# Optimization experiments

Measured on AMD Instinct MI355X. Metric: run time of the kernel, lower is better.

## Reference

```python
import jax, jax.numpy as jnp
import numpy as np

N = 50000
E = 800000
D_IN = 128
D_HID = 128
D_OUT = 64


def setup_inputs() -> dict:
    key = jax.random.key(0)
    ks = jax.random.split(key, 9)
    x = jax.random.normal(ks[0], (N, D_IN), dtype=jnp.float32)
    edge_index = jax.random.randint(ks[1], (2, E), 0, N, dtype=jnp.int64)
    # PyG SAGEConv params: lin_l (neighbor path, with bias), lin_r (root path, no bias)
    s1 = 1.0 / np.sqrt(D_IN)
    s2 = 1.0 / np.sqrt(D_HID)
    return {
        "x": x,
        "edge_index": edge_index,
        "W1l": jax.random.uniform(ks[2], (D_IN, D_HID), jnp.float32, -s1, s1),
        "b1": jax.random.uniform(ks[3], (D_HID,), jnp.float32, -s1, s1),
        "W1r": jax.random.uniform(ks[4], (D_IN, D_HID), jnp.float32, -s1, s1),
        "W2l": jax.random.uniform(ks[5], (D_HID, D_OUT), jnp.float32, -s2, s2),
        "b2": jax.random.uniform(ks[6], (D_OUT,), jnp.float32, -s2, s2),
        "W2r": jax.random.uniform(ks[7], (D_HID, D_OUT), jnp.float32, -s2, s2),
    }


def _sage_conv(h, src, dst, Wl, b, Wr, n_nodes):
    # mean-aggregate source features onto target nodes
    msg = h[src]  # [E, d] gather
    summed = jax.ops.segment_sum(msg, dst, num_segments=n_nodes)
    cnt = jax.ops.segment_sum(jnp.ones((src.shape[0],), h.dtype), dst, num_segments=n_nodes)
    mean = summed / jnp.maximum(cnt, 1.0)[:, None]
    return mean @ Wl + b + h @ Wr


def reference(x, edge_index, W1l, b1, W1r, W2l, b2, W2r):
    src, dst = edge_index[0], edge_index[1]
    n = x.shape[0]
    h = jax.nn.relu(_sage_conv(x, src, dst, W1l, b1, W1r, n))
    # dropout is identity in eval mode
    return _sage_conv(h, src, dst, W2l, b2, W2r, n)
```

## Files before the change

### kernel.cpp

```cpp
#include <hip/hip_runtime.h>

#define NN   50000
#define NE   800000
#define CAP  48
#define NPG  6250
#define EPB  3125
#define SEG  576

#define BIN_BLOCKS  256
#define CVT_BLOCKS  (3125 + 128)
#define ZERO_BLOCKS 196
#define SCAT_BLOCKS 2048

typedef __attribute__((ext_vector_type(8))) short bf16x8;
typedef __attribute__((ext_vector_type(4))) float f32x4;

__device__ __forceinline__ unsigned short f2b(float f) {
    unsigned int u = __builtin_bit_cast(unsigned int, f);
    u += 0x7FFFu + ((u >> 16) & 1u);
    return (unsigned short)(u >> 16);
}
__device__ __forceinline__ float b2f_lo(unsigned int u) {
    return __builtin_bit_cast(float, u << 16);
}
__device__ __forceinline__ float b2f_hi(unsigned int u) {
    return __builtin_bit_cast(float, u & 0xFFFF0000u);
}

__global__ __launch_bounds__(256) void prep_kernel(const int* __restrict__ src,
                                                   const int* __restrict__ dst,
                                                   int* __restrict__ bcnt,
                                                   unsigned* __restrict__ stage,
                                                   const float* __restrict__ x,
                                                   const float* __restrict__ W1l,
                                                   const float* __restrict__ W1r,
                                                   const float* __restrict__ W2l,
                                                   const float* __restrict__ W2r,
                                                   unsigned short* __restrict__ xb,
                                                   unsigned short* __restrict__ Bt1,
                                                   unsigned short* __restrict__ Bt2,
                                                   int* __restrict__ cursor) {
    if (blockIdx.x < BIN_BLOCKS) {
        __shared__ int cnt[16][8];
        __shared__ int repoff[16][8];
        const int tid = threadIdx.x;
        const int b   = blockIdx.x;
        const int r   = tid >> 4;
        if (tid < 128) ((int*)cnt)[tid] = 0;
        __syncthreads();

        unsigned recs[13], metas[13];
#pragma unroll
        for (int it = 0; it < 13; ++it) {
            const int i = it * 256 + tid;
            metas[it] = 0xFFFFFFFFu;
            if (i < EPB) {
                const int e = b * EPB + i;
                const int s = src[e], d = dst[e];
                const int g = d / NPG;
                const int dloc = d - g * NPG;
                const int slot = atomicAdd(&cnt[r][g], 1);
                recs[it]  = ((unsigned)dloc << 16) | (unsigned)s;
                metas[it] = ((unsigned)r << 20) | ((unsigned)g << 16) | (unsigned)slot;
            }
        }
        __syncthreads();
        if (tid < 8) {
            int off = 0;
#pragma unroll
            for (int rr = 0; rr < 16; ++rr) { repoff[rr][tid] = off; off += cnt[rr][tid]; }
            bcnt[tid * 256 + b] = off;
        }
        __syncthreads();
#pragma unroll
        for (int it = 0; it < 13; ++it) {
            if (metas[it] != 0xFFFFFFFFu) {
                const int rr   = metas[it] >> 20;
                const int g    = (metas[it] >> 16) & 7;
                const int slot = metas[it] & 0xFFFF;
                const int pos  = repoff[rr][g] + slot;
                if (pos < SEG) stage[((g << 8) + b) * SEG + pos] = recs[it];
            }
        }
    } else if (blockIdx.x < BIN_BLOCKS + 3125) {
        int i = (blockIdx.x - BIN_BLOCKS) * 256 + threadIdx.x;
        const float4* p = reinterpret_cast<const float4*>(x) + (size_t)i * 2;
        float4 a = p[0], b = p[1];
        uint4 u;
        u.x = (unsigned)f2b(a.x) | ((unsigned)f2b(a.y) << 16);
        u.y = (unsigned)f2b(a.z) | ((unsigned)f2b(a.w) << 16);
        u.z = (unsigned)f2b(b.x) | ((unsigned)f2b(b.y) << 16);
        u.w = (unsigned)f2b(b.z) | ((unsigned)f2b(b.w) << 16);
        reinterpret_cast<uint4*>(xb)[i] = u;
    } else if (blockIdx.x < BIN_BLOCKS + CVT_BLOCKS) {
        int t = (blockIdx.x - BIN_BLOCKS - 3125) * 256 + threadIdx.x;
        if (t < 32768) {
            int c = t >> 8, k = t & 255;
            float v = (k < 128) ? W1l[k * 128 + c] : W1r[(k - 128) * 128 + c];
            Bt1[c * 256 + k] = f2b(v);
        }
        if (t < 16384) {
            int c = t >> 7, k = t & 127;
            float v = (c < 64) ? W2l[k * 64 + c] : W2r[k * 64 + (c - 64)];
            Bt2[c * 128 + k] = f2b(v);
        }
    } else {
        int i = (blockIdx.x - BIN_BLOCKS - CVT_BLOCKS) * 256 + threadIdx.x;
        if (i < NN) cursor[i] = 0;
    }
}

__global__ __launch_bounds__(256) void scatter_kernel(const int* __restrict__ bcnt,
                                                      const unsigned* __restrict__ stage,
                                                      int* __restrict__ cursor,
                                                      int* __restrict__ col) {
    const int g = blockIdx.x & 7;
    const int b = blockIdx.x >> 3;
    int cnt = bcnt[g * 256 + b];
    if (cnt > SEG) cnt = SEG;
    const unsigned* sp = stage + (size_t)((g << 8) + b) * SEG;
    const int n0 = g * NPG;
    for (int i = threadIdx.x; i < cnt; i += 256) {
        unsigned rec = sp[i];
        int d = n0 + (int)(rec >> 16);
        int p = atomicAdd(&cursor[d], 1);
        if (p < CAP) col[d * CAP + p] = (int)(rec & 0xFFFFu);
    }
}

__global__ __launch_bounds__(256) void agg_gemm1(const unsigned short* __restrict__ xb,
                                                 const int* __restrict__ cursor,
                                                 const int* __restrict__ col,
                                                 const unsigned short* __restrict__ Bt1,
                                                 const float* __restrict__ bias,
                                                 unsigned short* __restrict__ hb) {
    constexpr int LDA = 264;
    __shared__ unsigned short As[64 * LDA];

    const int base = blockIdx.x * 64;
    const int tid  = threadIdx.x;
    const int l    = tid & 15;
    const int sub  = tid >> 4;

    const uint4* fp = reinterpret_cast<const uint4*>(xb);

    for (int gq = 0; gq < 4; ++gq) {
        const int r  = gq * 16 + sub;
        const int gn = base + r;
        float a0 = 0.f, a1 = 0.f, a2 = 0.f, a3 = 0.f,
              a4 = 0.f, a5 = 0.f, a6 = 0.f, a7 = 0.f;
        uint4 xrow = make_uint4(0, 0, 0, 0);
        if (gn < NN) {
            int len = cursor[gn];
            len = (len > CAP) ? CAP : len;
            const int4* cp = reinterpret_cast<const int4*>(col + gn * CAP);
            int j = 0;
            for (; j + 4 <= len; j += 4) {
                int4 c4 = cp[j >> 2];
                uint4 v0 = fp[c4.x * 16 + l];
                uint4 v1 = fp[c4.y * 16 + l];
                uint4 v2 = fp[c4.z * 16 + l];
                uint4 v3 = fp[c4.w * 16 + l];
                a0 += (b2f_lo(v0.x) + b2f_lo(v1.x)) + (b2f_lo(v2.x) + b2f_lo(v3.x));
                a1 += (b2f_hi(v0.x) + b2f_hi(v1.x)) + (b2f_hi(v2.x) + b2f_hi(v3.x));
                a2 += (b2f_lo(v0.y) + b2f_lo(v1.y)) + (b2f_lo(v2.y) + b2f_lo(v3.y));
                a3 += (b2f_hi(v0.y) + b2f_hi(v1.y)) + (b2f_hi(v2.y) + b2f_hi(v3.y));
                a4 += (b2f_lo(v0.z) + b2f_lo(v1.z)) + (b2f_lo(v2.z) + b2f_lo(v3.z));
                a5 += (b2f_hi(v0.z) + b2f_hi(v1.z)) + (b2f_hi(v2.z) + b2f_hi(v3.z));
                a6 += (b2f_lo(v0.w) + b2f_lo(v1.w)) + (b2f_lo(v2.w) + b2f_lo(v3.w));
                a7 += (b2f_hi(v0.w) + b2f_hi(v1.w)) + (b2f_hi(v2.w) + b2f_hi(v3.w));
            }
            for (; j < len; ++j) {
                uint4 v0 = fp[col[gn * CAP + j] * 16 + l];
                a0 += b2f_lo(v0.x);  a1 += b2f_hi(v0.x);
                a2 += b2f_lo(v0.y);  a3 += b2f_hi(v0.y);
                a4 += b2f_lo(v0.z);  a5 += b2f_hi(v0.z);
                a6 += b2f_lo(v0.w);  a7 += b2f_hi(v0.w);
            }
            const float inv = 1.0f / fmaxf((float)len, 1.0f);
            a0 *= inv; a1 *= inv; a2 *= inv; a3 *= inv;
            a4 *= inv; a5 *= inv; a6 *= inv; a7 *= inv;
            xrow = fp[gn * 16 + l];
        }
        uint4 u;
        u.x = (unsigned)f2b(a0) | ((unsigned)f2b(a1) << 16);
        u.y = (unsigned)f2b(a2) | ((unsigned)f2b(a3) << 16);
        u.z = (unsigned)f2b(a4) | ((unsigned)f2b(a5) << 16);
        u.w = (unsigned)f2b(a6) | ((unsigned)f2b(a7) << 16);
        *reinterpret_cast<uint4*>(&As[r * LDA + l * 8])       = u;
        *reinterpret_cast<uint4*>(&As[r * LDA + 128 + l * 8]) = xrow;
    }
    __syncthreads();

    const int wid  = tid >> 6, lane = tid & 63;
    const int lr   = lane & 15;
    const int lk   = (lane >> 4) * 8;

    f32x4 acc[4][2];
#pragma unroll
    for (int t = 0; t < 4; ++t) {
        acc[t][0] = (f32x4){0.f, 0.f, 0.f, 0.f};
        acc[t][1] = (f32x4){0.f, 0.f, 0.f, 0.f};
    }

    for (int ks = 0; ks < 8; ++ks) {
        const int k = ks * 32 + lk;
        bf16x8 b0 = *reinterpret_cast<const bf16x8*>(Bt1 + (size_t)(wid * 32 + lr) * 256 + k);
        bf16x8 b1 = *reinterpret_cast<const bf16x8*>(Bt1 + (size_t)(wid * 32 + 16 + lr) * 256 + k);
#pragma unroll
        for (int t = 0; t < 4; ++t) {
            bf16x8 a = *reinterpret_cast<const bf16x8*>(&As[(t * 16 + lr) * LDA + k]);
            acc[t][0] = __builtin_amdgcn_mfma_f32_16x16x32_bf16(a, b0, acc[t][0], 0, 0, 0);
            acc[t][1] = __builtin_amdgcn_mfma_f32_16x16x32_bf16(a, b1, acc[t][1], 0, 0, 0);
        }
    }

    const int ccol = lane & 15;
    const int ri   = (lane >> 4) * 4;
#pragma unroll
    for (int t = 0; t < 4; ++t) {
#pragma unroll
        for (int f = 0; f < 2; ++f) {
            const int colg = wid * 32 + f * 16 + ccol;
            const float bv = bias[colg];
#pragma unroll
            for (int i = 0; i < 4; ++i) {
                const int gn = base + t * 16 + ri + i;
                if (gn < NN) {
                    hb[(size_t)gn * 128 + colg] = f2b(fmaxf(acc[t][f][i] + bv, 0.f));
                }
            }
        }
    }
}

template <int DB>
__global__ __launch_bounds__(256) void agg_kernel(const unsigned short* __restrict__ feat,
                                                  const int* __restrict__ cursor,
                                                  const int* __restrict__ col,
                                                  float* outf) {
    constexpr int TPN = DB / 8;
    constexpr int NPB = 256 / TPN;
    const int n = blockIdx.x * NPB + threadIdx.x / TPN;
    const int l = threadIdx.x % TPN;
    if (n >= NN) return;
    int len = cursor[n];
    len = (len > CAP) ? CAP : len;
    float a0 = 0.f, a1 = 0.f, a2 = 0.f, a3 = 0.f, a4 = 0.f, a5 = 0.f, a6 = 0.f, a7 = 0.f;
    const uint4* fp = reinterpret_cast<const uint4*>(feat);
    const int4*  cp = reinterpret_cast<const int4*>(col + n * CAP);

    int j = 0;
    for (; j + 4 <= len; j += 4) {
        int4 c4 = cp[j >> 2];
        uint4 v0 = fp[c4.x * TPN + l];
        uint4 v1 = fp[c4.y * TPN + l];
        uint4 v2 = fp[c4.z * TPN + l];
        uint4 v3 = fp[c4.w * TPN + l];
        a0 += (b2f_lo(v0.x) + b2f_lo(v1.x)) + (b2f_lo(v2.x) + b2f_lo(v3.x));
        a1 += (b2f_hi(v0.x) + b2f_hi(v1.x)) + (b2f_hi(v2.x) + b2f_hi(v3.x));
        a2 += (b2f_lo(v0.y) + b2f_lo(v1.y)) + (b2f_lo(v2.y) + b2f_lo(v3.y));
        a3 += (b2f_hi(v0.y) + b2f_hi(v1.y)) + (b2f_hi(v2.y) + b2f_hi(v3.y));
        a4 += (b2f_lo(v0.z) + b2f_lo(v1.z)) + (b2f_lo(v2.z) + b2f_lo(v3.z));
        a5 += (b2f_hi(v0.z) + b2f_hi(v1.z)) + (b2f_hi(v2.z) + b2f_hi(v3.z));
        a6 += (b2f_lo(v0.w) + b2f_lo(v1.w)) + (b2f_lo(v2.w) + b2f_lo(v3.w));
        a7 += (b2f_hi(v0.w) + b2f_hi(v1.w)) + (b2f_hi(v2.w) + b2f_hi(v3.w));
    }
    for (; j < len; ++j) {
        uint4 v0 = fp[col[n * CAP + j] * TPN + l];
        a0 += b2f_lo(v0.x);  a1 += b2f_hi(v0.x);
        a2 += b2f_lo(v0.y);  a3 += b2f_hi(v0.y);
        a4 += b2f_lo(v0.z);  a5 += b2f_hi(v0.z);
        a6 += b2f_lo(v0.w);  a7 += b2f_hi(v0.w);
    }
    const float inv = 1.0f / fmaxf((float)len, 1.0f);
    a0 *= inv; a1 *= inv; a2 *= inv; a3 *= inv;
    a4 *= inv; a5 *= inv; a6 *= inv; a7 *= inv;
    const float4* ap = reinterpret_cast<const float4*>(outf + (size_t)n * DB) + l * 2;
    float4 b0 = ap[0], b1 = ap[1];
    float4 o0 = make_float4(a0 + b0.x, a1 + b0.y, a2 + b0.z, a3 + b0.w);
    float4 o1 = make_float4(a4 + b1.x, a5 + b1.y, a6 + b1.z, a7 + b1.w);
    float4* op = reinterpret_cast<float4*>(outf + (size_t)n * DB) + l * 2;
    op[0] = o0; op[1] = o1;
}

__global__ __launch_bounds__(256) void gemm2_kernel(const unsigned short* __restrict__ A0,
                                                    const unsigned short* __restrict__ Bt,
                                                    const float* __restrict__ bias,
                                                    unsigned short* __restrict__ outb,
                                                    float* __restrict__ outf) {
    constexpr int K   = 128;
    constexpr int LDK = K + 8;
    __shared__ unsigned short Bs[128 * LDK];

    const int tid = threadIdx.x;
    for (int idx = tid; idx < 128 * (K / 8); idx += 256) {
        int c = idx / (K / 8), kc = idx % (K / 8);
        uint4 v = *reinterpret_cast<const uint4*>(Bt + (size_t)c * K + kc * 8);
        *reinterpret_cast<uint4*>(&Bs[c * LDK + kc * 8]) = v;
    }
    __syncthreads();

    const int base = blockIdx.x * 64;
    const int wid  = tid >> 6, lane = tid & 63;
    const int lr   = lane & 15;
    const int lk   = (lane >> 4) * 8;

    f32x4 acc[4][2];
#pragma unroll
    for (int t = 0; t < 4; ++t) {
        acc[t][0] = (f32x4){0.f, 0.f, 0.f, 0.f};
        acc[t][1] = (f32x4){0.f, 0.f, 0.f, 0.f};
    }

    for (int ks = 0; ks < K / 32; ++ks) {
        const int k = ks * 32 + lk;
        bf16x8 b0 = *reinterpret_cast<const bf16x8*>(&Bs[(wid * 32 + lr) * LDK + k]);
        bf16x8 b1 = *reinterpret_cast<const bf16x8*>(&Bs[(wid * 32 + 16 + lr) * LDK + k]);
#pragma unroll
        for (int t = 0; t < 4; ++t) {
            const int row = base + t * 16 + lr;
            uint4 av = make_uint4(0, 0, 0, 0);
            if (row < NN) av = *reinterpret_cast<const uint4*>(A0 + (size_t)row * 128 + k);
            bf16x8 a = *reinterpret_cast<const bf16x8*>(&av);
            acc[t][0] = __builtin_amdgcn_mfma_f32_16x16x32_bf16(a, b0, acc[t][0], 0, 0, 0);
            acc[t][1] = __builtin_amdgcn_mfma_f32_16x16x32_bf16(a, b1, acc[t][1], 0, 0, 0);
        }
    }

    const int ccol = lane & 15;
    const int ri   = (lane >> 4) * 4;
#pragma unroll
    for (int t = 0; t < 4; ++t) {
#pragma unroll
        for (int f = 0; f < 2; ++f) {
            const int colg = wid * 32 + f * 16 + ccol;
#pragma unroll
            for (int i = 0; i < 4; ++i) {
                const int gn = base + t * 16 + ri + i;
                if (gn < NN) {
                    float v = acc[t][f][i];
                    if (colg < 64) outb[(size_t)gn * 64 + colg] = f2b(v);
                    else           outf[(size_t)gn * 64 + (colg - 64)] = v + bias[colg - 64];
                }
            }
        }
    }
}

extern "C" void kernel_launch(void* const* d_in, const int* in_sizes, int n_in,
                              void* d_out, int out_size, void* d_ws, size_t ws_size,
                              hipStream_t stream) {
    const float* x   = (const float*)d_in[0];
    const int*   ei  = (const int*)d_in[1];
    const float* W1l = (const float*)d_in[2];
    const float* b1  = (const float*)d_in[3];
    const float* W1r = (const float*)d_in[4];
    const float* W2l = (const float*)d_in[5];
    const float* b2  = (const float*)d_in[6];
    const float* W2r = (const float*)d_in[7];

    const int* src = ei;
    const int* dst = ei + NE;

    char* ws = (char*)d_ws;
    int* cursor = (int*)ws;
    int* bcnt   = (int*)(ws + 200000);
    int* col    = (int*)(ws + 208384);
    unsigned short* xb  = (unsigned short*)(ws + 9808384);
    unsigned short* hlb = (unsigned short*)(ws + 22608384);
    unsigned short* hb  = (unsigned short*)(ws + 35408384);
    unsigned*       stage = (unsigned*)(ws + 35408384);
    unsigned short* Bt1 = (unsigned short*)(ws + 48208384);
    unsigned short* Bt2 = (unsigned short*)(ws + 48273920);
    float* outp = (float*)d_out;

    prep_kernel<<<BIN_BLOCKS + CVT_BLOCKS + ZERO_BLOCKS, 256, 0, stream>>>(
        src, dst, bcnt, stage, x, W1l, W1r, W2l, W2r, xb, Bt1, Bt2, cursor);
    scatter_kernel<<<SCAT_BLOCKS, 256, 0, stream>>>(bcnt, stage, cursor, col);

    agg_gemm1<<<(NN + 63) / 64, 256, 0, stream>>>(xb, cursor, col, Bt1, b1, hb);

    gemm2_kernel<<<(NN + 63) / 64, 256, 0, stream>>>(hb, Bt2, b2, hlb, outp);
    agg_kernel<64><<<(NN * 8 + 255) / 256, 256, 0, stream>>>(hlb, cursor, col, outp);
}
```

Measured before the change: 130.2 us.

## Fuse second-layer GEMM into first aggregation+GEMM kernel via shared-memory hidden tile

The layer-1 hidden activations are no longer written to global memory. Each block converts its ReLU output to bf16 in shared memory, reusing the A tile buffer, and immediately multiplies it by the layer-2 weights. The layer-2 neighbour-path and root-path outputs are written directly to their destinations. This removes one kernel launch and a global round trip of the hidden tensor. In exchange it adds two block barriers and reads the second weight matrix from global memory instead of from a shared-memory copy.

Measured after the change: 118.3 us. -9.2%, faster.

```diff
diff --git a/kernel.cpp b/kernel.cpp
--- a/kernel.cpp
+++ b/kernel.cpp
@@ -128,13 +128,17 @@
     }
 }
 
-__global__ __launch_bounds__(256) void agg_gemm1(const unsigned short* __restrict__ xb,
-                                                 const int* __restrict__ cursor,
-                                                 const int* __restrict__ col,
-                                                 const unsigned short* __restrict__ Bt1,
-                                                 const float* __restrict__ bias,
-                                                 unsigned short* __restrict__ hb) {
+__global__ __launch_bounds__(256) void agg_gemm12(const unsigned short* __restrict__ xb,
+                                                  const int* __restrict__ cursor,
+                                                  const int* __restrict__ col,
+                                                  const unsigned short* __restrict__ Bt1,
+                                                  const unsigned short* __restrict__ Bt2,
+                                                  const float* __restrict__ b1,
+                                                  const float* __restrict__ b2,
+                                                  unsigned short* __restrict__ hlb,
+                                                  float* __restrict__ outp) {
     constexpr int LDA = 264;
+    constexpr int LDH = 136;
     __shared__ unsigned short As[64 * LDA];
 
     const int base = blockIdx.x * 64;
@@ -195,6 +199,8 @@
     const int wid  = tid >> 6, lane = tid & 63;
     const int lr   = lane & 15;
     const int lk   = (lane >> 4) * 8;
+    const int ccol = lane & 15;
+    const int ri   = (lane >> 4) * 4;
 
     f32x4 acc[4][2];
 #pragma unroll
@@ -202,7 +208,6 @@
         acc[t][0] = (f32x4){0.f, 0.f, 0.f, 0.f};
         acc[t][1] = (f32x4){0.f, 0.f, 0.f, 0.f};
     }
-
     for (int ks = 0; ks < 8; ++ks) {
         const int k = ks * 32 + lk;
         bf16x8 b0 = *reinterpret_cast<const bf16x8*>(Bt1 + (size_t)(wid * 32 + lr) * 256 + k);
@@ -214,20 +219,53 @@
             acc[t][1] = __builtin_amdgcn_mfma_f32_16x16x32_bf16(a, b1, acc[t][1], 0, 0, 0);
         }
     }
-
-    const int ccol = lane & 15;
-    const int ri   = (lane >> 4) * 4;
+    __syncthreads();
+
+    unsigned short* Hs = As;
 #pragma unroll
     for (int t = 0; t < 4; ++t) {
 #pragma unroll
         for (int f = 0; f < 2; ++f) {
             const int colg = wid * 32 + f * 16 + ccol;
-            const float bv = bias[colg];
+            const float bv = b1[colg];
+#pragma unroll
+            for (int i = 0; i < 4; ++i) {
+                Hs[(t * 16 + ri + i) * LDH + colg] = f2b(fmaxf(acc[t][f][i] + bv, 0.f));
+            }
+        }
+    }
+    __syncthreads();
+
+    f32x4 acc2[4][2];
+#pragma unroll
+    for (int t = 0; t < 4; ++t) {
+        acc2[t][0] = (f32x4){0.f, 0.f, 0.f, 0.f};
+        acc2[t][1] = (f32x4){0.f, 0.f, 0.f, 0.f};
+    }
+    for (int ks = 0; ks < 4; ++ks) {
+        const int k = ks * 32 + lk;
+        bf16x8 b0 = *reinterpret_cast<const bf16x8*>(Bt2 + (size_t)(wid * 32 + lr) * 128 + k);
+        bf16x8 b1 = *reinterpret_cast<const bf16x8*>(Bt2 + (size_t)(wid * 32 + 16 + lr) * 128 + k);
+#pragma unroll
+        for (int t = 0; t < 4; ++t) {
+            bf16x8 a = *reinterpret_cast<const bf16x8*>(&Hs[(t * 16 + lr) * LDH + k]);
+            acc2[t][0] = __builtin_amdgcn_mfma_f32_16x16x32_bf16(a, b0, acc2[t][0], 0, 0, 0);
+            acc2[t][1] = __builtin_amdgcn_mfma_f32_16x16x32_bf16(a, b1, acc2[t][1], 0, 0, 0);
+        }
+    }
+
+#pragma unroll
+    for (int t = 0; t < 4; ++t) {
+#pragma unroll
+        for (int f = 0; f < 2; ++f) {
+            const int colg = wid * 32 + f * 16 + ccol;
 #pragma unroll
             for (int i = 0; i < 4; ++i) {
                 const int gn = base + t * 16 + ri + i;
                 if (gn < NN) {
-                    hb[(size_t)gn * 128 + colg] = f2b(fmaxf(acc[t][f][i] + bv, 0.f));
+                    float v = acc2[t][f][i];
+                    if (colg < 64) hlb[(size_t)gn * 64 + colg] = f2b(v);
+                    else           outp[(size_t)gn * 64 + (colg - 64)] = v + b2[colg - 64];
                 }
             }
         }
@@ -284,70 +322,6 @@
     op[0] = o0; op[1] = o1;
 }
 
-__global__ __launch_bounds__(256) void gemm2_kernel(const unsigned short* __restrict__ A0,
-                                                    const unsigned short* __restrict__ Bt,
-                                                    const float* __restrict__ bias,
-                                                    unsigned short* __restrict__ outb,
-                                                    float* __restrict__ outf) {
-    constexpr int K   = 128;
-    constexpr int LDK = K + 8;
-    __shared__ unsigned short Bs[128 * LDK];
-
-    const int tid = threadIdx.x;
-    for (int idx = tid; idx < 128 * (K / 8); idx += 256) {
-        int c = idx / (K / 8), kc = idx % (K / 8);
-        uint4 v = *reinterpret_cast<const uint4*>(Bt + (size_t)c * K + kc * 8);
-        *reinterpret_cast<uint4*>(&Bs[c * LDK + kc * 8]) = v;
-    }
-    __syncthreads();
-
-    const int base = blockIdx.x * 64;
-    const int wid  = tid >> 6, lane = tid & 63;
-    const int lr   = lane & 15;
-    const int lk   = (lane >> 4) * 8;
-
-    f32x4 acc[4][2];
-#pragma unroll
-    for (int t = 0; t < 4; ++t) {
-        acc[t][0] = (f32x4){0.f, 0.f, 0.f, 0.f};
-        acc[t][1] = (f32x4){0.f, 0.f, 0.f, 0.f};
-    }
-
-    for (int ks = 0; ks < K / 32; ++ks) {
-        const int k = ks * 32 + lk;
-        bf16x8 b0 = *reinterpret_cast<const bf16x8*>(&Bs[(wid * 32 + lr) * LDK + k]);
-        bf16x8 b1 = *reinterpret_cast<const bf16x8*>(&Bs[(wid * 32 + 16 + lr) * LDK + k]);
-#pragma unroll
-        for (int t = 0; t < 4; ++t) {
-            const int row = base + t * 16 + lr;
-            uint4 av = make_uint4(0, 0, 0, 0);
-            if (row < NN) av = *reinterpret_cast<const uint4*>(A0 + (size_t)row * 128 + k);
-            bf16x8 a = *reinterpret_cast<const bf16x8*>(&av);
-            acc[t][0] = __builtin_amdgcn_mfma_f32_16x16x32_bf16(a, b0, acc[t][0], 0, 0, 0);
-            acc[t][1] = __builtin_amdgcn_mfma_f32_16x16x32_bf16(a, b1, acc[t][1], 0, 0, 0);
-        }
-    }
-
-    const int ccol = lane & 15;
-    const int ri   = (lane >> 4) * 4;
-#pragma unroll
-    for (int t = 0; t < 4; ++t) {
-#pragma unroll
-        for (int f = 0; f < 2; ++f) {
-            const int colg = wid * 32 + f * 16 + ccol;
-#pragma unroll
-            for (int i = 0; i < 4; ++i) {
-                const int gn = base + t * 16 + ri + i;
-                if (gn < NN) {
-                    float v = acc[t][f][i];
-                    if (colg < 64) outb[(size_t)gn * 64 + colg] = f2b(v);
-                    else           outf[(size_t)gn * 64 + (colg - 64)] = v + bias[colg - 64];
-                }
-            }
-        }
-    }
-}
-
 extern "C" void kernel_launch(void* const* d_in, const int* in_sizes, int n_in,
                               void* d_out, int out_size, void* d_ws, size_t ws_size,
                               hipStream_t stream) {
@@ -369,7 +343,6 @@
     int* col    = (int*)(ws + 208384);
     unsigned short* xb  = (unsigned short*)(ws + 9808384);
     unsigned short* hlb = (unsigned short*)(ws + 22608384);
-    unsigned short* hb  = (unsigned short*)(ws + 35408384);
     unsigned*       stage = (unsigned*)(ws + 35408384);
     unsigned short* Bt1 = (unsigned short*)(ws + 48208384);
     unsigned short* Bt2 = (unsigned short*)(ws + 48273920);
@@ -379,8 +352,8 @@
         src, dst, bcnt, stage, x, W1l, W1r, W2l, W2r, xb, Bt1, Bt2, cursor);
     scatter_kernel<<<SCAT_BLOCKS, 256, 0, stream>>>(bcnt, stage, cursor, col);
 
-    agg_gemm1<<<(NN + 63) / 64, 256, 0, stream>>>(xb, cursor, col, Bt1, b1, hb);
-
-    gemm2_kernel<<<(NN + 63) / 64, 256, 0, stream>>>(hb, Bt2, b2, hlb, outp);
+    agg_gemm12<<<(NN + 63) / 64, 256, 0, stream>>>(xb, cursor, col, Bt1, Bt2,
+                                                   b1, b2, hlb, outp);
+
     agg_kernel<64><<<(NN * 8 + 255) / 256, 256, 0, stream>>>(hlb, cursor, col, outp);
 }
```
